# Kernel tuning notes

Hardware: AMD Instinct MI355X
Metric: run time of the kernel (lower is better)

## Reference

```python
import jax, jax.numpy as jnp
import numpy as np

B, S, D, H, FF, L = 32, 512, 512, 16, 2048, 3
DH = D // H
EPS = 1e-3


def setup_inputs() -> dict:
    key = jax.random.key(0)
    ks = jax.random.split(key, 8)
    sc = 0.02
    n = lambda k, shp: (jax.random.normal(k, shp, jnp.float32) * sc)
    return {
        "input_seq": jax.random.normal(ks[0], (B, S, D), jnp.float32),
        "Wq": n(ks[1], (L, D, D)), "bq": jnp.zeros((L, D), jnp.float32),
        "Wk": n(ks[2], (L, D, D)), "bk": jnp.zeros((L, D), jnp.float32),
        "Wv": n(ks[3], (L, D, D)), "bv": jnp.zeros((L, D), jnp.float32),
        "g1": jnp.ones((L, D), jnp.float32), "be1": jnp.zeros((L, D), jnp.float32),
        "W1": n(ks[4], (L, D, FF)), "b1": jnp.zeros((L, FF), jnp.float32),
        "W2": n(ks[5], (L, FF, D)), "b2": jnp.zeros((L, D), jnp.float32),
        "g2": jnp.ones((L, D), jnp.float32), "be2": jnp.zeros((L, D), jnp.float32),
    }


def batch_norm(x, g, b):
    # training-mode BatchNorm1d over channels=last dim; stats over (batch, seq)
    m = jnp.mean(x, axis=(0, 1))
    v = jnp.var(x, axis=(0, 1))  # biased, as torch BN uses for normalization
    return (x - m) * jax.lax.rsqrt(v + EPS) * g + b


def encoder_fwd(x, Wq, bq, Wk, bk, Wv, bv, g1, be1, W1, b1, W2, b2, g2, be2):
    scale = 1.0 / jnp.sqrt(jnp.float32(DH))
    for i in range(L):
        # --- multi-head attention block ---
        q = jax.nn.relu(x @ Wq[i] + bq[i]).reshape(B, S, H, DH)
        k = jax.nn.relu(x @ Wk[i] + bk[i]).reshape(B, S, H, DH)
        v = jax.nn.relu(x @ Wv[i] + bv[i]).reshape(B, S, H, DH)
        scores = jnp.einsum("bshd,bthd->bhst", q, k) * scale
        attn = jax.nn.softmax(scores, axis=-1)  # dropout = identity (eval)
        o = jnp.einsum("bhst,bthd->bshd", attn, v).reshape(B, S, D)
        x = batch_norm(o + x, g1[i], be1[i])
        # --- feed-forward block ---
        h = jax.nn.relu(x @ W1[i] + b1[i])
        x = batch_norm(h @ W2[i] + b2[i] + x, g2[i], be2[i])
    return x


def reference(input_seq, Wq, bq, Wk, bk, Wv, bv, g1, be1, W1, b1, W2, b2, g2, be2):
    return encoder_fwd(input_seq, Wq, bq, Wk, bk, Wv, bv, g1, be1, W1, b1, W2, b2, g2, be2)
```

## Files before the change

### kernel.cpp

```cpp
#include <hip/hip_runtime.h>
#include <hip/hip_bf16.h>

typedef __bf16 bf16;
typedef __bf16 bf16x2 __attribute__((ext_vector_type(2)));
typedef __bf16 bf16x4 __attribute__((ext_vector_type(4)));
typedef __bf16 bf16x8 __attribute__((ext_vector_type(8)));
typedef float f32x4 __attribute__((ext_vector_type(4)));

#define SEQ 512
#define DIM 512
#define NH 16
#define DH 32
#define FFD 2048
#define NBATCH 32
#define MTOT (NBATCH * SEQ)

__device__ __forceinline__ void gl_lds16(const bf16* g, bf16* l) {
  __builtin_amdgcn_global_load_lds(
      (const __attribute__((address_space(1))) void*)g,
      (__attribute__((address_space(3))) void*)l, 16, 0, 0);
}

template <int BM, int MF, int EPI>
__global__ __launch_bounds__(512, 2)
void gemm8p(const bf16* __restrict__ A, const bf16* __restrict__ BT,
            const float* __restrict__ bias0, const float* __restrict__ bias1,
            const float* __restrict__ bias2,
            bf16* __restrict__ out0, bf16* __restrict__ out1, bf16* __restrict__ out2,
            int N, int K, int NBX) {
  __shared__ bf16 As[2][BM * 64];
  __shared__ bf16 Bs[2][256 * 64];
  const int tid = threadIdx.x, lane = tid & 63, wave = tid >> 6;
  const int wm = wave >> 2, wn = wave & 3;
  const int lo = lane & 15, hi = lane >> 4;
  const int nwg = gridDim.x;
  const int bid = (blockIdx.x & 7) * (nwg >> 3) + (blockIdx.x >> 3);
  const int bn0 = (bid % NBX) * 256;
  const int bm0 = (bid / NBX) * BM;
  const bf16* Ab = A + (size_t)bm0 * K;
  const bf16* Bb = BT + (size_t)bn0 * K;
  constexpr int AL = BM / 64;
  constexpr int MH = MF / 2;

  auto STAGE = [&](int d, int k0) {
#pragma unroll
    for (int q = 0; q < AL; ++q) {
      const int bi = q * 512 + tid;
      const int r = bi >> 3;
      const int ce = ((bi & 7) ^ (r & 7)) * 8;
      gl_lds16(Ab + (size_t)r * K + k0 + ce, &As[d][bi * 8]);
    }
#pragma unroll
    for (int q = 0; q < 4; ++q) {
      const int bi = q * 512 + tid;
      const int r = bi >> 3;
      const int ce = ((bi & 7) ^ (r & 7)) * 8;
      gl_lds16(Bb + (size_t)r * K + k0 + ce, &Bs[d][bi * 8]);
    }
  };

  f32x4 acc[MF][4] = {};
  bf16x8 afr[MH][2], bfr[2][2];

  auto rdA = [&](const bf16* as, int half) {
#pragma unroll
    for (int i = 0; i < MH; ++i)
#pragma unroll
      for (int ks = 0; ks < 2; ++ks) {
        const int r = wm * (MF * 16) + (half * MH + i) * 16 + lo;
        const int cb = (ks * 64 + hi * 16) ^ ((lo & 7) << 4);
        afr[i][ks] = *(const bf16x8*)((const char*)as + r * 128 + cb);
      }
  };
  auto rdB = [&](const bf16* bs, int np) {
#pragma unroll
    for (int j = 0; j < 2; ++j)
#pragma unroll
      for (int ks = 0; ks < 2; ++ks) {
        const int r = wn * 64 + (np * 2 + j) * 16 + lo;
        const int cb = (ks * 64 + hi * 16) ^ ((lo & 7) << 4);
        bfr[j][ks] = *(const bf16x8*)((const char*)bs + r * 128 + cb);
      }
  };
  auto mma = [&](int half, int np) {
    __builtin_amdgcn_s_setprio(1);
#pragma unroll
    for (int i = 0; i < MH; ++i)
#pragma unroll
      for (int j = 0; j < 2; ++j)
#pragma unroll
        for (int ks = 0; ks < 2; ++ks)
          acc[half * MH + i][np * 2 + j] = __builtin_amdgcn_mfma_f32_16x16x32_bf16(
              afr[i][ks], bfr[j][ks], acc[half * MH + i][np * 2 + j], 0, 0, 0);
    __builtin_amdgcn_s_setprio(0);
  };

  const int NT = K >> 6;
  STAGE(0, 0);
  int cur = 0;
  for (int t = 0; t < NT; ++t) {
    const bf16* as = As[cur];
    const bf16* bs = Bs[cur];
    if (t + 1 < NT) {
      STAGE(cur ^ 1, (t + 1) << 6);
      if constexpr (AL == 4) asm volatile("s_waitcnt vmcnt(8)" ::: "memory");
      else                   asm volatile("s_waitcnt vmcnt(6)" ::: "memory");
    } else {
      asm volatile("s_waitcnt vmcnt(0)" ::: "memory");
    }
    asm volatile("s_barrier" ::: "memory");
    rdA(as, 0); rdB(bs, 0); mma(0, 0);
    asm volatile("s_barrier" ::: "memory");
    rdB(bs, 1); mma(0, 1);
    asm volatile("s_barrier" ::: "memory");
    rdA(as, 1); rdB(bs, 0); mma(1, 0);
    asm volatile("s_barrier" ::: "memory");
    rdB(bs, 1); mma(1, 1);
    asm volatile("s_barrier" ::: "memory");
    cur ^= 1;
  }
#pragma unroll
  for (int i = 0; i < MF; ++i) {
    const int m = bm0 + wm * (MF * 16) + i * 16 + hi * 4;
#pragma unroll
    for (int j = 0; j < 4; ++j) {
      const int n = bn0 + wn * 64 + j * 16 + lo;
      if constexpr (EPI == 0) {
        const int part = n >> 9, c = n & 511;
        const int h_ = c >> 5, dh_ = c & 31;
        const float bs = (part == 0 ? bias0 : part == 1 ? bias1 : bias2)[c];
        const int b_ = m >> 9, s_ = m & 511;
        if (part < 2) {
          bf16* dst = part == 0 ? out0 : out1;
#pragma unroll
          for (int r = 0; r < 4; ++r)
            dst[(((size_t)(b_ * NH + h_)) * SEQ + s_ + r) * DH + dh_] =
                (bf16)fmaxf(acc[i][j][r] + bs, 0.f);
        } else {
          bf16x4 vv;
#pragma unroll
          for (int r = 0; r < 4; ++r) vv[r] = (bf16)fmaxf(acc[i][j][r] + bs, 0.f);
          *(bf16x4*)&out2[(((size_t)(b_ * NH + h_)) * DH + dh_) * SEQ + s_] = vv;
        }
      } else {
        const float bs = bias0[n];
#pragma unroll
        for (int r = 0; r < 4; ++r) {
          float v = acc[i][j][r] + bs;
          if constexpr (EPI == 1) v = fmaxf(v, 0.f);
          out0[(size_t)(m + r) * N + n] = (bf16)v;
        }
      }
    }
  }
}

__global__ __launch_bounds__(512, 2)
void attn_kernel(const bf16* __restrict__ Qb, const bf16* __restrict__ Kb,
                 const bf16* __restrict__ Vt, bf16* __restrict__ O) {
  __shared__ bf16 Ks[512][40];
  __shared__ bf16 Vs[32][520];
  __shared__ bf16 P[8][16][136];
  const int bh = blockIdx.x;
  const int tid = threadIdx.x, lane = tid & 63, wave = tid >> 6;
  const int lo = lane & 15, hi = lane >> 4;
  const bf16* Qp = Qb + (size_t)bh * SEQ * DH;
  const bf16* Kp = Kb + (size_t)bh * SEQ * DH;
  const bf16* Vp = Vt + (size_t)bh * DH * SEQ;
  for (int idx = tid; idx < 2048; idx += 512) {
    const int row = idx >> 2, seg = idx & 3;
    *(bf16x8*)&Ks[row][seg * 8] = *(const bf16x8*)(Kp + row * DH + seg * 8);
  }
  for (int idx = tid; idx < 2048; idx += 512) {
    const int row = idx >> 6, c16 = idx & 63;
    *(bf16x8*)&Vs[row][c16 * 8] = *(const bf16x8*)(Vp + row * SEQ + c16 * 8);
  }
  __syncthreads();
  const float CEXP = 0.17677669529663687f * 1.44269504088896f;
  const int b_ = bh >> 4, h_ = bh & 15;
  for (int c = wave; c < 32; c += 8) {
    const int s0 = c * 16;
    const bf16x8 qf = *(const bf16x8*)(Qp + (s0 + lo) * DH + hi * 8);
    float sm[4] = {0.f, 0.f, 0.f, 0.f};
    f32x4 o0 = {0.f, 0.f, 0.f, 0.f}, o1 = {0.f, 0.f, 0.f, 0.f};
#pragma unroll
    for (int q4 = 0; q4 < 4; ++q4) {
      f32x4 acc[8];
      __builtin_amdgcn_s_setprio(1);
#pragma unroll
      for (int t = 0; t < 8; ++t) {
        const bf16x8 kf = *(const bf16x8*)&Ks[q4 * 128 + t * 16 + lo][hi * 8];
        acc[t] = __builtin_amdgcn_mfma_f32_16x16x32_bf16(qf, kf, (f32x4){0.f, 0.f, 0.f, 0.f}, 0, 0, 0);
      }
      __builtin_amdgcn_s_setprio(0);
#pragma unroll
      for (int t = 0; t < 8; ++t)
#pragma unroll
        for (int j = 0; j < 4; ++j) {
          const float p = __builtin_amdgcn_exp2f(acc[t][j] * CEXP);
          acc[t][j] = p; sm[j] += p;
        }
#pragma unroll
      for (int t = 0; t < 8; ++t)
#pragma unroll
        for (int j = 0; j < 4; ++j)
          P[wave][hi * 4 + j][t * 16 + lo] = (bf16)acc[t][j];
      __builtin_amdgcn_s_setprio(1);
#pragma unroll
      for (int kkl = 0; kkl < 4; ++kkl) {
        const bf16x8 pa  = *(const bf16x8*)&P[wave][lo][kkl * 32 + hi * 8];
        const bf16x8 vf0 = *(const bf16x8*)&Vs[lo][q4 * 128 + kkl * 32 + hi * 8];
        const bf16x8 vf1 = *(const bf16x8*)&Vs[16 + lo][q4 * 128 + kkl * 32 + hi * 8];
        o0 = __builtin_amdgcn_mfma_f32_16x16x32_bf16(pa, vf0, o0, 0, 0, 0);
        o1 = __builtin_amdgcn_mfma_f32_16x16x32_bf16(pa, vf1, o1, 0, 0, 0);
      }
      __builtin_amdgcn_s_setprio(0);
    }
#pragma unroll
    for (int d = 1; d < 16; d <<= 1)
#pragma unroll
      for (int j = 0; j < 4; ++j) sm[j] += __shfl_xor(sm[j], d);
#pragma unroll
    for (int j = 0; j < 4; ++j) {
      const float inv = 1.f / sm[j];
      const int s_ = s0 + hi * 4 + j;
      const size_t base = ((size_t)(b_ * SEQ + s_)) * DIM + h_ * DH;
      O[base + lo]      = (bf16)(o0[j] * inv);
      O[base + 16 + lo] = (bf16)(o1[j] * inv);
    }
  }
}

__global__ __launch_bounds__(256)
void cast_kernel(const float* __restrict__ in, bf16* __restrict__ out) {
  const size_t i = ((size_t)blockIdx.x * 256 + threadIdx.x) * 4;
  const float4 v = *(const float4*)(in + i);
  bf16x4 o;
  o[0] = (bf16)v.x; o[1] = (bf16)v.y; o[2] = (bf16)v.z; o[3] = (bf16)v.w;
  *(bf16x4*)(out + i) = o;
}

__global__ __launch_bounds__(256)
void transpose_cast(const float* __restrict__ W, bf16* __restrict__ WT, int K, int N,
                    size_t dstLayerStride) {
  __shared__ float t[32][33];
  const int l = blockIdx.z;
  const float* Wl = W + (size_t)l * K * N;
  bf16* WTl = WT + (size_t)l * dstLayerStride;
  const int n0 = blockIdx.x * 32, k0 = blockIdx.y * 32;
  const int tx = threadIdx.x, ty = threadIdx.y;
#pragma unroll
  for (int r = 0; r < 32; r += 8)
    t[ty + r][tx] = Wl[(size_t)(k0 + ty + r) * N + n0 + tx];
  __syncthreads();
#pragma unroll
  for (int r = 0; r < 32; r += 8)
    WTl[(size_t)(n0 + ty + r) * K + k0 + tx] = (bf16)t[tx][ty + r];
}

__global__ __launch_bounds__(256)
void bn_stats(const bf16* __restrict__ o, const bf16* __restrict__ x,
              float* __restrict__ part) {
  __shared__ float redS[4][64][8];
  __shared__ float redQ[4][64][8];
  const int tid = threadIdx.x, blk = blockIdx.x;
  const int cg = tid & 63, rs = tid >> 6;
  float s[8] = {}, q[8] = {};
#pragma unroll 4
  for (int k = 0; k < 16; ++k) {
    const size_t idx = ((size_t)blk * 64 + rs + k * 4) * DIM + cg * 8;
    const bf16x8 ov = *(const bf16x8*)(o + idx);
    const bf16x8 xv = *(const bf16x8*)(x + idx);
#pragma unroll
    for (int j = 0; j < 8; ++j) {
      const float a = (float)ov[j] + (float)xv[j];
      s[j] += a; q[j] += a * a;
    }
  }
#pragma unroll
  for (int j = 0; j < 8; ++j) { redS[rs][cg][j] = s[j]; redQ[rs][cg][j] = q[j]; }
  __syncthreads();
  if (tid < 64) {
#pragma unroll
    for (int j = 0; j < 8; ++j) {
      const float ss = redS[0][tid][j] + redS[1][tid][j] + redS[2][tid][j] + redS[3][tid][j];
      const float qq = redQ[0][tid][j] + redQ[1][tid][j] + redQ[2][tid][j] + redQ[3][tid][j];
      float2 w = {ss, qq};
      ((float2*)part)[(size_t)blk * DIM + tid * 8 + j] = w;
    }
  }
}

__global__ __launch_bounds__(256)
void bn_finalize(const float* __restrict__ part, const float* __restrict__ g,
                 const float* __restrict__ be, float* __restrict__ coef) {
  const int c = blockIdx.x * 256 + threadIdx.x;
  float s = 0, q = 0;
  for (int b = 0; b < 256; ++b) {
    const float2 p = ((const float2*)part)[(size_t)b * DIM + c];
    s += p.x; q += p.y;
  }
  const float inv_n = 1.f / (float)MTOT;
  const float mean = s * inv_n;
  const float var = q * inv_n - mean * mean;
  const float k = g[c] * rsqrtf(var + 1e-3f);
  coef[c] = k;
  coef[DIM + c] = be[c] - mean * k;
}

__global__ __launch_bounds__(256)
void bn_apply(const bf16* __restrict__ o, const bf16* __restrict__ x,
              const float* __restrict__ coef, bf16* __restrict__ xout,
              float* __restrict__ fout) {
  const size_t i = ((size_t)blockIdx.x * 256 + threadIdx.x) * 8;
  const int c = (int)(i & (DIM - 1));
  const bf16x8 ov = *(const bf16x8*)(o + i);
  const bf16x8 xv = *(const bf16x8*)(x + i);
  float y[8];
#pragma unroll
  for (int j = 0; j < 8; ++j)
    y[j] = ((float)ov[j] + (float)xv[j]) * coef[c + j] + coef[DIM + c + j];
  if (fout) {
    float4 a = {y[0], y[1], y[2], y[3]};
    float4 b = {y[4], y[5], y[6], y[7]};
    *(float4*)(fout + i) = a;
    *(float4*)(fout + i + 4) = b;
  } else {
    bf16x8 yb;
#pragma unroll
    for (int j = 0; j < 8; ++j) yb[j] = (bf16)y[j];
    *(bf16x8*)(xout + i) = yb;
  }
}

#define OFF_XB   ((size_t)0)
#define OFF_Q    ((size_t)16777216)
#define OFF_K    ((size_t)33554432)
#define OFF_V    ((size_t)50331648)
#define OFF_O    ((size_t)67108864)
#define OFF_H    ((size_t)16777216)
#define OFF_Z    ((size_t)83886080)
#define OFF_QKVT ((size_t)100663296)
#define OFF_W1T  ((size_t)105381888)
#define OFF_W2T  ((size_t)111673344)
#define OFF_PART ((size_t)117964800)
#define OFF_COEF ((size_t)119013376)

extern "C" void kernel_launch(void* const* d_in, const int* in_sizes, int n_in,
                              void* d_out, int out_size, void* d_ws, size_t ws_size,
                              hipStream_t stream) {
  const float* x_in = (const float*)d_in[0];
  const float* Wq = (const float*)d_in[1];
  const float* bq = (const float*)d_in[2];
  const float* Wk = (const float*)d_in[3];
  const float* bk = (const float*)d_in[4];
  const float* Wv = (const float*)d_in[5];
  const float* bv = (const float*)d_in[6];
  const float* g1 = (const float*)d_in[7];
  const float* be1 = (const float*)d_in[8];
  const float* W1 = (const float*)d_in[9];
  const float* b1 = (const float*)d_in[10];
  const float* W2 = (const float*)d_in[11];
  const float* b2 = (const float*)d_in[12];
  const float* g2 = (const float*)d_in[13];
  const float* be2 = (const float*)d_in[14];
  float* out = (float*)d_out;

  char* ws = (char*)d_ws;
  bf16* xb   = (bf16*)(ws + OFF_XB);
  bf16* qb   = (bf16*)(ws + OFF_Q);
  bf16* kb   = (bf16*)(ws + OFF_K);
  bf16* vb   = (bf16*)(ws + OFF_V);
  bf16* ob   = (bf16*)(ws + OFF_O);
  bf16* hb   = (bf16*)(ws + OFF_H);
  bf16* zb   = (bf16*)(ws + OFF_Z);
  bf16* qkvT = (bf16*)(ws + OFF_QKVT);
  bf16* w1T  = (bf16*)(ws + OFF_W1T);
  bf16* w2T  = (bf16*)(ws + OFF_W2T);
  float* part = (float*)(ws + OFF_PART);
  float* coef = (float*)(ws + OFF_COEF);

  const dim3 blk32(32, 8);
  transpose_cast<<<dim3(16, 16, 3), blk32, 0, stream>>>(Wq, qkvT,              512, 512, 1536 * 512);
  transpose_cast<<<dim3(16, 16, 3), blk32, 0, stream>>>(Wk, qkvT + 512 * 512,  512, 512, 1536 * 512);
  transpose_cast<<<dim3(16, 16, 3), blk32, 0, stream>>>(Wv, qkvT + 1024 * 512, 512, 512, 1536 * 512);
  transpose_cast<<<dim3(64, 16, 3), blk32, 0, stream>>>(W1, w1T, 512, 2048, 2048 * 512);
  transpose_cast<<<dim3(16, 64, 3), blk32, 0, stream>>>(W2, w2T, 2048, 512, 512 * 2048);
  cast_kernel<<<8192, 256, 0, stream>>>(x_in, xb);

  for (int l = 0; l < 3; ++l) {
    const bf16* qkvT_l = qkvT + (size_t)l * 1536 * 512;
    gemm8p<128, 4, 0><<<768, 512, 0, stream>>>(
        xb, qkvT_l, bq + l * 512, bk + l * 512, bv + l * 512, qb, kb, vb, 1536, 512, 6);
    attn_kernel<<<512, 512, 0, stream>>>(qb, kb, vb, ob);
    bn_stats<<<256, 256, 0, stream>>>(ob, xb, part);
    bn_finalize<<<2, 256, 0, stream>>>(part, g1 + l * 512, be1 + l * 512, coef);
    bn_apply<<<4096, 256, 0, stream>>>(ob, xb, coef, xb, nullptr);
    gemm8p<256, 8, 1><<<512, 512, 0, stream>>>(
        xb, w1T + (size_t)l * 2048 * 512, b1 + l * 2048, nullptr, nullptr,
        hb, nullptr, nullptr, 2048, 512, 8);
    gemm8p<128, 4, 2><<<256, 512, 0, stream>>>(
        hb, w2T + (size_t)l * 512 * 2048, b2 + l * 512, nullptr, nullptr,
        zb, nullptr, nullptr, 512, 2048, 2);
    bn_stats<<<256, 256, 0, stream>>>(zb, xb, part);
    bn_finalize<<<2, 256, 0, stream>>>(part, g2 + l * 512, be2 + l * 512, coef);
    if (l < 2)
      bn_apply<<<4096, 256, 0, stream>>>(zb, xb, coef, xb, nullptr);
    else
      bn_apply<<<4096, 256, 0, stream>>>(zb, xb, coef, nullptr, out);
  }
}
```

Before: 897.6 us.

## Restructure GEMM tiles to 256-row blocks with staged prefetch interleaved into MFMA phases

Replaces the gemm8p kernel with gemm9, which fixes the M tile at 256 rows and makes the N tile and wave grid template parameters. The QKV and W2 GEMMs now use 256x128 tiles, and FFN1 keeps 256x256. The next K-tile's global-to-LDS loads are split into chunks and issued between MFMA phases instead of all at once, and each phase loads all B fragments and runs a wider MFMA block. The aim is better overlap of memory loads with compute and fewer barriers per phase. In exchange the tile shapes change per GEMM and the hand-set vmcnt waits must match the new chunking.

```diff
diff --git a/kernel.cpp b/kernel.cpp
--- a/kernel.cpp
+++ b/kernel.cpp
@@ -21,107 +21,106 @@
       (__attribute__((address_space(3))) void*)l, 16, 0, 0);
 }
 
-template <int BM, int MF, int EPI>
+template <int WM, int WN, int EPI>
 __global__ __launch_bounds__(512, 2)
-void gemm8p(const bf16* __restrict__ A, const bf16* __restrict__ BT,
-            const float* __restrict__ bias0, const float* __restrict__ bias1,
-            const float* __restrict__ bias2,
-            bf16* __restrict__ out0, bf16* __restrict__ out1, bf16* __restrict__ out2,
-            int N, int K, int NBX) {
-  __shared__ bf16 As[2][BM * 64];
-  __shared__ bf16 Bs[2][256 * 64];
+void gemm9(const bf16* __restrict__ A, const bf16* __restrict__ BT,
+           const float* __restrict__ bias0, const float* __restrict__ bias1,
+           const float* __restrict__ bias2,
+           bf16* __restrict__ out0, bf16* __restrict__ out1, bf16* __restrict__ out2,
+           int N, int K, int NBX) {
+  constexpr int BN  = WN * 64;
+  constexpr int MFR = 16 / WM;
+  constexpr int PH  = MFR / 2;
+  constexpr int TL  = 4 + WN;
+  constexpr int CH  = TL / PH;
+  __shared__ bf16 As[2][256 * 64];
+  __shared__ bf16 Bs[2][BN * 64];
   const int tid = threadIdx.x, lane = tid & 63, wave = tid >> 6;
-  const int wm = wave >> 2, wn = wave & 3;
+  const int wm = wave / WN, wn = wave % WN;
   const int lo = lane & 15, hi = lane >> 4;
   const int nwg = gridDim.x;
   const int bid = (blockIdx.x & 7) * (nwg >> 3) + (blockIdx.x >> 3);
-  const int bn0 = (bid % NBX) * 256;
-  const int bm0 = (bid / NBX) * BM;
+  const int bn0 = (bid % NBX) * BN;
+  const int bm0 = (bid / NBX) * 256;
   const bf16* Ab = A + (size_t)bm0 * K;
   const bf16* Bb = BT + (size_t)bn0 * K;
-  constexpr int AL = BM / 64;
-  constexpr int MH = MF / 2;
-
-  auto STAGE = [&](int d, int k0) {
-#pragma unroll
-    for (int q = 0; q < AL; ++q) {
-      const int bi = q * 512 + tid;
-      const int r = bi >> 3;
+
+  auto STAGE1 = [&](int d, int k0, int q) {
+    if (q < 4) {
+      const int bi = q * 512 + tid, r = bi >> 3;
       const int ce = ((bi & 7) ^ (r & 7)) * 8;
       gl_lds16(Ab + (size_t)r * K + k0 + ce, &As[d][bi * 8]);
-    }
-#pragma unroll
-    for (int q = 0; q < 4; ++q) {
-      const int bi = q * 512 + tid;
-      const int r = bi >> 3;
+    } else {
+      const int bi = (q - 4) * 512 + tid, r = bi >> 3;
       const int ce = ((bi & 7) ^ (r & 7)) * 8;
       gl_lds16(Bb + (size_t)r * K + k0 + ce, &Bs[d][bi * 8]);
     }
   };
 
-  f32x4 acc[MF][4] = {};
-  bf16x8 afr[MH][2], bfr[2][2];
-
-  auto rdA = [&](const bf16* as, int half) {
-#pragma unroll
-    for (int i = 0; i < MH; ++i)
-#pragma unroll
-      for (int ks = 0; ks < 2; ++ks) {
-        const int r = wm * (MF * 16) + (half * MH + i) * 16 + lo;
-        const int cb = (ks * 64 + hi * 16) ^ ((lo & 7) << 4);
-        afr[i][ks] = *(const bf16x8*)((const char*)as + r * 128 + cb);
-      }
-  };
-  auto rdB = [&](const bf16* bs, int np) {
-#pragma unroll
-    for (int j = 0; j < 2; ++j)
-#pragma unroll
-      for (int ks = 0; ks < 2; ++ks) {
-        const int r = wn * 64 + (np * 2 + j) * 16 + lo;
-        const int cb = (ks * 64 + hi * 16) ^ ((lo & 7) << 4);
-        bfr[j][ks] = *(const bf16x8*)((const char*)bs + r * 128 + cb);
-      }
-  };
-  auto mma = [&](int half, int np) {
-    __builtin_amdgcn_s_setprio(1);
-#pragma unroll
-    for (int i = 0; i < MH; ++i)
-#pragma unroll
-      for (int j = 0; j < 2; ++j)
-#pragma unroll
-        for (int ks = 0; ks < 2; ++ks)
-          acc[half * MH + i][np * 2 + j] = __builtin_amdgcn_mfma_f32_16x16x32_bf16(
-              afr[i][ks], bfr[j][ks], acc[half * MH + i][np * 2 + j], 0, 0, 0);
-    __builtin_amdgcn_s_setprio(0);
-  };
-
+  f32x4 acc[MFR][4] = {};
+  bf16x8 bfr[4][2];
   const int NT = K >> 6;
-  STAGE(0, 0);
+#pragma unroll
+  for (int q = 0; q < TL; ++q) STAGE1(0, 0, q);
   int cur = 0;
   for (int t = 0; t < NT; ++t) {
     const bf16* as = As[cur];
     const bf16* bs = Bs[cur];
+    const int nk0 = (t + 1) << 6;
     if (t + 1 < NT) {
-      STAGE(cur ^ 1, (t + 1) << 6);
-      if constexpr (AL == 4) asm volatile("s_waitcnt vmcnt(8)" ::: "memory");
-      else                   asm volatile("s_waitcnt vmcnt(6)" ::: "memory");
+#pragma unroll
+      for (int q = 0; q < CH; ++q) STAGE1(cur ^ 1, nk0, q);
+      if constexpr (CH == 2) asm volatile("s_waitcnt vmcnt(2)" ::: "memory");
+      else                   asm volatile("s_waitcnt vmcnt(3)" ::: "memory");
     } else {
       asm volatile("s_waitcnt vmcnt(0)" ::: "memory");
     }
     asm volatile("s_barrier" ::: "memory");
-    rdA(as, 0); rdB(bs, 0); mma(0, 0);
-    asm volatile("s_barrier" ::: "memory");
-    rdB(bs, 1); mma(0, 1);
-    asm volatile("s_barrier" ::: "memory");
-    rdA(as, 1); rdB(bs, 0); mma(1, 0);
-    asm volatile("s_barrier" ::: "memory");
-    rdB(bs, 1); mma(1, 1);
-    asm volatile("s_barrier" ::: "memory");
+#pragma unroll
+    for (int p = 0; p < PH; ++p) {
+      bf16x8 afr[2][2];
+      if (p == 0) {
+#pragma unroll
+        for (int j = 0; j < 4; ++j)
+#pragma unroll
+          for (int ks = 0; ks < 2; ++ks) {
+            const int r = wn * 64 + j * 16 + lo;
+            const int cb = (ks * 64 + hi * 16) ^ ((lo & 7) << 4);
+            bfr[j][ks] = *(const bf16x8*)((const char*)bs + r * 128 + cb);
+          }
+      }
+#pragma unroll
+      for (int i = 0; i < 2; ++i)
+#pragma unroll
+        for (int ks = 0; ks < 2; ++ks) {
+          const int r = wm * (MFR * 16) + (p * 2 + i) * 16 + lo;
+          const int cb = (ks * 64 + hi * 16) ^ ((lo & 7) << 4);
+          afr[i][ks] = *(const bf16x8*)((const char*)as + r * 128 + cb);
+        }
+      if (t + 1 < NT && p < PH - 1) {
+#pragma unroll
+        for (int q = (p + 1) * CH; q < (p + 2) * CH; ++q) STAGE1(cur ^ 1, nk0, q);
+      }
+      asm volatile("s_barrier" ::: "memory");
+      asm volatile("s_waitcnt lgkmcnt(0)" ::: "memory");
+      __builtin_amdgcn_sched_barrier(0);
+      __builtin_amdgcn_s_setprio(1);
+#pragma unroll
+      for (int i = 0; i < 2; ++i)
+#pragma unroll
+        for (int j = 0; j < 4; ++j)
+#pragma unroll
+          for (int ks = 0; ks < 2; ++ks)
+            acc[p * 2 + i][j] = __builtin_amdgcn_mfma_f32_16x16x32_bf16(
+                afr[i][ks], bfr[j][ks], acc[p * 2 + i][j], 0, 0, 0);
+      __builtin_amdgcn_s_setprio(0);
+      asm volatile("s_barrier" ::: "memory");
+    }
     cur ^= 1;
   }
 #pragma unroll
-  for (int i = 0; i < MF; ++i) {
-    const int m = bm0 + wm * (MF * 16) + i * 16 + hi * 4;
+  for (int i = 0; i < MFR; ++i) {
+    const int m = bm0 + wm * (MFR * 16) + i * 16 + hi * 4;
 #pragma unroll
     for (int j = 0; j < 4; ++j) {
       const int n = bn0 + wn * 64 + j * 16 + lo;
@@ -390,18 +389,18 @@
 
   for (int l = 0; l < 3; ++l) {
     const bf16* qkvT_l = qkvT + (size_t)l * 1536 * 512;
-    gemm8p<128, 4, 0><<<768, 512, 0, stream>>>(
-        xb, qkvT_l, bq + l * 512, bk + l * 512, bv + l * 512, qb, kb, vb, 1536, 512, 6);
+    gemm9<4, 2, 0><<<768, 512, 0, stream>>>(
+        xb, qkvT_l, bq + l * 512, bk + l * 512, bv + l * 512, qb, kb, vb, 1536, 512, 12);
     attn_kernel<<<512, 512, 0, stream>>>(qb, kb, vb, ob);
     bn_stats<<<256, 256, 0, stream>>>(ob, xb, part);
     bn_finalize<<<2, 256, 0, stream>>>(part, g1 + l * 512, be1 + l * 512, coef);
     bn_apply<<<4096, 256, 0, stream>>>(ob, xb, coef, xb, nullptr);
-    gemm8p<256, 8, 1><<<512, 512, 0, stream>>>(
+    gemm9<2, 4, 1><<<512, 512, 0, stream>>>(
         xb, w1T + (size_t)l * 2048 * 512, b1 + l * 2048, nullptr, nullptr,
         hb, nullptr, nullptr, 2048, 512, 8);
-    gemm8p<128, 4, 2><<<256, 512, 0, stream>>>(
+    gemm9<4, 2, 2><<<256, 512, 0, stream>>>(
         hb, w2T + (size_t)l * 512 * 2048, b2 + l * 512, nullptr, nullptr,
-        zb, nullptr, nullptr, 512, 2048, 2);
+        zb, nullptr, nullptr, 512, 2048, 4);
     bn_stats<<<256, 256, 0, stream>>>(zb, xb, part);
     bn_finalize<<<2, 256, 0, stream>>>(part, g2 + l * 512, be2 + l * 512, coef);
     if (l < 2)
```

Measured after the change: 877.2 us. 1.02x faster.
